# Kernel tuning notes

Measured on AMD Instinct MI355X. Metric: run time of the kernel, lower is better.

The kernel has to match this reference:

```python
import jax, jax.numpy as jnp
import numpy as np

SIZE_DICT = 512
DIM_DICT = 256
TEMPERATURE = 0.5
EPS = 1e-10


def setup_inputs() -> dict:
    key = jax.random.key(0)
    k1, k2, k3 = jax.random.split(key, 3)
    bs, dim_z, W, H = 32, DIM_DICT, 32, 32
    z_from_encoder = jax.random.normal(k1, (bs, dim_z, W, H), dtype=jnp.float32)
    kappa_q = jnp.ones((1,), dtype=jnp.float32)
    codebook = jax.random.normal(k2, (SIZE_DICT, DIM_DICT), dtype=jnp.float32)
    gumbel_u = jax.random.uniform(k3, (bs * W * H, SIZE_DICT), dtype=jnp.float32)
    return {"z_from_encoder": z_from_encoder, "kappa_q": kappa_q,
            "codebook": codebook, "gumbel_u": gumbel_u, "flg_train": 1}


def reference(z_from_encoder, kappa_q, codebook, gumbel_u, flg_train):
    bs, dim_z, W, H = z_from_encoder.shape
    # [bs, dim_z, W, H] -> [bs*W*H, dim_z]
    z_flat = jnp.transpose(z_from_encoder, (0, 2, 3, 1)).reshape(-1, dim_z)
    kq = jnp.clip(kappa_q, 1e-5, 1e5)  # scalar-ish [1]
    # L2-normalize codebook rows
    cb = codebook / jnp.linalg.norm(codebook, axis=1, keepdims=True)
    # logit = -distance = kappa * <z, c>   [N, K]
    logit = kq * (z_flat @ cb.T)
    logit = logit - jnp.max(logit, axis=-1, keepdims=True)
    logit = jnp.clip(logit, -50.0, 50.0)
    probabilities = jax.nn.softmax(logit, axis=-1)
    log_probabilities = jax.nn.log_softmax(logit, axis=-1)
    # training path: gumbel-softmax relaxation
    g = -jnp.log(-jnp.log(gumbel_u + EPS) + EPS)
    encodings = jax.nn.softmax((logit + g) / TEMPERATURE, axis=-1)
    z_quantized = (encodings @ cb).reshape(bs, W, H, dim_z)
    avg_probs = jnp.mean(jax.lax.stop_gradient(probabilities), axis=0)
    z_to_decoder = jnp.transpose(z_quantized, (0, 3, 1, 2))
    kld_discrete = jnp.sum(probabilities * log_probabilities) / bs
    kld_continuous = jnp.mean(
        jnp.sum(z_from_encoder * (z_from_encoder - z_to_decoder) * kq[0],
                axis=(1, 2, 3)))
    loss = kld_discrete + kld_continuous
    avg_probs = jnp.clip(avg_probs, 1e-10, None)
    perplexity = jnp.exp(-jnp.sum(avg_probs * jnp.log(avg_probs + 1e-10)))
    return z_to_decoder, loss, perplexity
```

## Files before the change

### kernel.cpp

```cpp
#include <hip/hip_runtime.h>
#include <stdint.h>


typedef float v4f __attribute__((ext_vector_type(4)));
typedef short v8s __attribute__((ext_vector_type(8)));
typedef short v4s __attribute__((ext_vector_type(4)));

#define ZA_STR 264
#define L2_STR 520

__device__ __forceinline__ uint16_t f2bf(float x) {
  uint32_t u = __float_as_uint(x);
  u = u + 0x7fffu + ((u >> 16) & 1u);
  return (uint16_t)(u >> 16);
}


__global__ __launch_bounds__(256) void vq_prep(const float* __restrict__ cb,
                                               const float* __restrict__ kappa,
                                               char* __restrict__ ws) {
  const int b = blockIdx.x, t = threadIdx.x;
  uint16_t* cbn2 = (uint16_t*)ws;
  uint16_t* cbt2 = (uint16_t*)(ws + 262144);
  float* shadow  = (float*)(ws + 524288);
  float* scal    = (float*)(ws + 557056);
  __shared__ float s_rn[8];

  const int cbase = (b & 63) << 3;
  const int cl = t >> 5, lt = t & 31;
  const float4 f0 = *(const float4*)(cb + (cbase + cl) * 256 + lt * 8);
  const float4 f1 = *(const float4*)(cb + (cbase + cl) * 256 + lt * 8 + 4);
  float s = f0.x*f0.x + f0.y*f0.y + f0.z*f0.z + f0.w*f0.w
          + f1.x*f1.x + f1.y*f1.y + f1.z*f1.z + f1.w*f1.w;
#pragma unroll
  for (int mm = 1; mm < 32; mm <<= 1) s += __shfl_xor(s, mm, 64);
  if (lt == 0) s_rn[cl] = 1.0f / sqrtf(s);
  __syncthreads();

  union { v8s v; uint16_t u[8]; } pk;
  if (b < 64) {
    const float kq = fminf(fmaxf(kappa[0], 1e-5f), 1e5f);
    const int code = cbase + cl, dch = lt;
    const float rn = s_rn[cl] * kq;
    pk.u[0] = f2bf(f0.x * rn); pk.u[1] = f2bf(f0.y * rn);
    pk.u[2] = f2bf(f0.z * rn); pk.u[3] = f2bf(f0.w * rn);
    pk.u[4] = f2bf(f1.x * rn); pk.u[5] = f2bf(f1.y * rn);
    pk.u[6] = f2bf(f1.z * rn); pk.u[7] = f2bf(f1.w * rn);
    const int w = code >> 7, ct = (code >> 4) & 7, mcol = code & 15;
    const int ks = dch >> 2, q3 = dch & 3;
    *(v8s*)(cbn2 + ((ks * 8 + ct) * 4 + w) * 512 + (q3 * 16 + mcol) * 8) = pk.v;
  } else {
    const int cgroup = b - 64, d = t;
#pragma unroll
    for (int j = 0; j < 8; j++) {
      const int c = cbase + j;
      pk.u[j] = f2bf(cb[c * 256 + d] * s_rn[j]);
    }
    const int cc = cgroup >> 2, qq = cgroup & 3;
    const int wd = d >> 6, nt = (d >> 4) & 3, md = d & 15;
    *(v8s*)(cbt2 + ((cc * 4 + nt) * 4 + wd) * 512 + (qq * 16 + md) * 8) = pk.v;
    if (t < 128) shadow[(cgroup << 7) + t] = 0.f;
    if (cgroup == 0 && t >= 128 && t < 131) scal[t - 128] = 0.f;
  }
}

__global__ __launch_bounds__(256, 4) void vq_main(const float* __restrict__ z,
                                                  const float* __restrict__ gum,
                                                  char* __restrict__ ws,
                                                  float* __restrict__ out) {
  __shared__ char s_A[33280];
  __shared__ float s_pm[128], s_pS[128], s_pT[128];
  __shared__ float s_M[32], s_rS[32], s_kd[32], s_rSe[32], s_red[8];
  __shared__ float s_se[128], s_ce[128];
  __shared__ float s_col[512];

  const int t = threadIdx.x;
  const int w = t >> 6, lane = t & 63, q = lane >> 4, m = lane & 15;
  const int bi = blockIdx.x, b = bi >> 5, wh0 = (bi & 31) << 5;
  const int R0 = bi << 5;

  const uint16_t* cbn2 = (const uint16_t*)ws;
  const uint16_t* cbt2 = (const uint16_t*)(ws + 262144);
  float* shadow = (float*)(ws + 524288);
  float* scal   = (float*)(ws + 557056);

  uint16_t* za  = (uint16_t*)s_A;
  uint16_t* l2s = (uint16_t*)s_A;

  {
    float zs = 0.f;
    const int whb = (t & 7) << 2, dT = t >> 3;
    const float* zb = z + ((size_t)b << 18) + wh0 + whb;
#pragma unroll
    for (int s = 0; s < 8; s++) {
      const int d = dT + (s << 5);
      const float4 v = *(const float4*)(zb + (d << 10));
      zs += v.x * v.x + v.y * v.y + v.z * v.z + v.w * v.w;
      za[(whb + 0) * ZA_STR + d] = f2bf(v.x);
      za[(whb + 1) * ZA_STR + d] = f2bf(v.y);
      za[(whb + 2) * ZA_STR + d] = f2bf(v.z);
      za[(whb + 3) * ZA_STR + d] = f2bf(v.w);
    }
#pragma unroll
    for (int mm = 1; mm < 64; mm <<= 1) zs += __shfl_xor(zs, mm, 64);
    if (lane == 0) s_red[w] = zs;
  }
  __syncthreads();
  if (t == 0) atomicAdd(&scal[1], s_red[0] + s_red[1] + s_red[2] + s_red[3]);

  v4f acc0[8], acc1[8];
#pragma unroll
  for (int i = 0; i < 8; i++) { acc0[i] = (v4f)0.f; acc1[i] = (v4f)0.f; }
  {
    const uint16_t* bp  = cbn2 + (w << 9) + (lane << 3);
    const uint16_t* a0p = za + m * ZA_STR;
    const uint16_t* a1p = za + (m + 16) * ZA_STR;
#pragma unroll
    for (int ks = 0; ks < 8; ks++) {
      const v8s a0 = *(const v8s*)(a0p + (ks << 5) + (q << 3));
      const v8s a1 = *(const v8s*)(a1p + (ks << 5) + (q << 3));
#pragma unroll
      for (int ct = 0; ct < 8; ct++) {
        const v8s bf = *(const v8s*)(bp + (((ks << 3) + ct) << 11));
        acc0[ct] = __builtin_amdgcn_mfma_f32_16x16x32_bf16(a0, bf, acc0[ct], 0, 0, 0);
        acc1[ct] = __builtin_amdgcn_mfma_f32_16x16x32_bf16(a1, bf, acc1[ct], 0, 0, 0);
      }
    }
  }

  {
    auto stats_half = [&](v4f (&acc)[8], int half) {
#pragma unroll
      for (int reg = 0; reg < 4; reg++) {
        float mx = -1e30f;
#pragma unroll
        for (int ct = 0; ct < 8; ct++) mx = fmaxf(mx, acc[ct][reg]);
#pragma unroll
        for (int mm = 1; mm < 16; mm <<= 1) mx = fmaxf(mx, __shfl_xor(mx, mm, 64));
        float S = 0.f, T = 0.f;
#pragma unroll
        for (int ct = 0; ct < 8; ct++) {
          const float d = acc[ct][reg] - mx;
          const float e = __expf(d);
          S += e; T += d * e;
        }
#pragma unroll
        for (int mm = 1; mm < 16; mm <<= 1) { S += __shfl_xor(S, mm, 64); T += __shfl_xor(T, mm, 64); }
        if (m == 0) {
          const int r = half * 16 + q * 4 + reg;
          s_pm[(w << 5) + r] = mx; s_pS[(w << 5) + r] = S; s_pT[(w << 5) + r] = T;
        }
      }
    };
    stats_half(acc0, 0);
    stats_half(acc1, 1);
  }

  const float* gT = gum + (((size_t)R0 + (q << 2)) << 9) + (w << 7) + m;
  float gb[2][8];
#pragma unroll
  for (int ct = 0; ct < 8; ct++) gb[0][ct] = gT[ct << 4];
#pragma unroll
  for (int ct = 0; ct < 8; ct++) gb[1][ct] = gT[512 + (ct << 4)];

  __syncthreads();
  if (t < 32) {
    float M = s_pm[t];
    M = fmaxf(M, s_pm[32 + t]); M = fmaxf(M, s_pm[64 + t]); M = fmaxf(M, s_pm[96 + t]);
    float S = 0.f, T = 0.f;
#pragma unroll
    for (int ww = 0; ww < 4; ww++) {
      const float dm = s_pm[ww * 32 + t] - M;
      const float al = __expf(dm);
      S += s_pS[ww * 32 + t] * al;
      T += (s_pT[ww * 32 + t] + dm * s_pS[ww * 32 + t]) * al;
    }
    const float rS = 1.0f / S;
    s_M[t] = M; s_rS[t] = rS; s_kd[t] = T * rS - __logf(S);
  }
  __syncthreads();

  {
    const int c0 = w << 7;
    float colacc[8];
#pragma unroll
    for (int i = 0; i < 8; i++) colacc[i] = 0.f;
#pragma unroll
    for (int g = 0; g < 8; g++) {
      const int h = g >> 2, rg = g & 3;
      const int r = (h << 4) + (q << 2) + rg;
      const float Mr = s_M[r], rSr = s_rS[r];
      uint16_t* lrow = l2s + r * L2_STR + c0 + m;
      float se = 0.f, ce = 0.f;
#pragma unroll
      for (int ct = 0; ct < 8; ct++) {
        const float a = h ? acc1[ct][rg] : acc0[ct][rg];
        const float d = fmaxf(a - Mr, -50.0f);
        const float e = __expf(d);
        colacc[ct] += e * rSr;
        const float L = 1e-10f - __logf(gb[g & 1][ct] + 1e-10f);
        const float f = __fdividef(e, L);
        const float er = f * f;
        se += er;
        ce += er * (d + Mr);
        lrow[ct << 4] = f2bf(er);
      }
      if (g < 6) {
        const int g2 = g + 2;
        const int off = (((g2 >> 2) << 4) + (g2 & 3)) << 9;
#pragma unroll
        for (int ct = 0; ct < 8; ct++) gb[g & 1][ct] = gT[off + (ct << 4)];
      }
#pragma unroll
      for (int mm = 1; mm < 16; mm <<= 1) {
        se += __shfl_xor(se, mm, 64);
        ce += __shfl_xor(ce, mm, 64);
      }
      if (m == 0) { s_se[(w << 5) + r] = se; s_ce[(w << 5) + r] = ce; }
    }
#pragma unroll
    for (int i = 0; i < 8; i++) {
      colacc[i] += __shfl_xor(colacc[i], 16, 64);
      colacc[i] += __shfl_xor(colacc[i], 32, 64);
    }
    if (q == 0) {
#pragma unroll
      for (int i = 0; i < 8; i++) s_col[c0 + (i << 4) + m] = colacc[i];
    }
  }
  __syncthreads();

  if (t < 32) {
    const float se = s_se[t] + s_se[32 + t] + s_se[64 + t] + s_se[96 + t];
    const float ce = s_ce[t] + s_ce[32 + t] + s_ce[64 + t] + s_ce[96 + t];
    s_rSe[t] = 1.0f / se;
    float cr = ce / se;
#pragma unroll
    for (int mm = 1; mm < 32; mm <<= 1) cr += __shfl_xor(cr, mm, 64);
    if (t == 0) atomicAdd(&scal[2], cr);
  }

  v4f acc2a[4], acc2b[4];
#pragma unroll
  for (int i = 0; i < 4; i++) { acc2a[i] = (v4f)0.f; acc2b[i] = (v4f)0.f; }
  {
    const uint16_t* a0p = l2s + m * L2_STR;
    const uint16_t* a1p = l2s + (m + 16) * L2_STR;
#pragma unroll
    for (int cc = 0; cc < 16; cc++) {
      const v8s a0 = *(const v8s*)(a0p + (cc << 5) + (q << 3));
      const v8s a1 = *(const v8s*)(a1p + (cc << 5) + (q << 3));
      const uint16_t* bp2 = cbt2 + (cc << 13) + (w << 9) + (lane << 3);
#pragma unroll
      for (int nt = 0; nt < 4; nt++) {
        const v8s bf = *(const v8s*)(bp2 + (nt << 11));
        acc2a[nt] = __builtin_amdgcn_mfma_f32_16x16x32_bf16(a0, bf, acc2a[nt], 0, 0, 0);
        acc2b[nt] = __builtin_amdgcn_mfma_f32_16x16x32_bf16(a1, bf, acc2b[nt], 0, 0, 0);
      }
    }
  }
  __syncthreads();

  {
    float* ob = out + ((size_t)b << 18) + wh0;
    const int d0 = w << 6;
    float rsA[4], rsB[4];
#pragma unroll
    for (int reg = 0; reg < 4; reg++) {
      rsA[reg] = s_rSe[q * 4 + reg];
      rsB[reg] = s_rSe[16 + q * 4 + reg];
    }
#pragma unroll
    for (int nt = 0; nt < 4; nt++) {
      const int d = d0 + (nt << 4) + m;
#pragma unroll
      for (int reg = 0; reg < 4; reg++) {
        ob[(d << 10) + q * 4 + reg]      = acc2a[nt][reg] * rsA[reg];
        ob[(d << 10) + 16 + q * 4 + reg] = acc2b[nt][reg] * rsB[reg];
      }
    }
  }

  {
    float* sh = shadow + ((bi & 15) << 9);
    atomicAdd(&sh[t], s_col[t]);
    atomicAdd(&sh[256 + t], s_col[256 + t]);
    if (w == 0) {
      float kd = s_kd[lane & 31];
#pragma unroll
      for (int mm = 1; mm < 64; mm <<= 1) kd += __shfl_xor(kd, mm, 64);
      if (lane == 0) atomicAdd(&scal[0], 0.5f * kd);
    }
  }
}

__global__ __launch_bounds__(512) void vq_final(const float* __restrict__ kappa,
                                                char* __restrict__ ws,
                                                float* __restrict__ out) {
  __shared__ float red[8];
  const int t = threadIdx.x;
  const float* shadow = (const float*)(ws + 524288);
  const float* scal   = (const float*)(ws + 557056);
  float s = 0.f;
#pragma unroll
  for (int j = 0; j < 16; j++) s += shadow[(j << 9) + t];
  float avg = fmaxf(s * (1.0f / 32768.0f), 1e-10f);
  float term = avg * __logf(avg + 1e-10f);
#pragma unroll
  for (int mm = 1; mm < 64; mm <<= 1) term += __shfl_xor(term, mm, 64);
  if ((t & 63) == 0) red[t >> 6] = term;
  __syncthreads();
  if (t == 0) {
    float H = 0.f;
#pragma unroll
    for (int i = 0; i < 8; i++) H += red[i];
    const float perpl = __expf(-H);
    const float kq = fminf(fmaxf(kappa[0], 1e-5f), 1e5f);
    const float loss = (scal[0] + kq * scal[1] - scal[2]) * (1.0f / 32.0f);
    out[8388608] = loss;
    out[8388609] = perpl;
  }
}

extern "C" void kernel_launch(void* const* d_in, const int* in_sizes, int n_in,
                              void* d_out, int out_size, void* d_ws, size_t ws_size,
                              hipStream_t stream) {
  const float* z     = (const float*)d_in[0];
  const float* kappa = (const float*)d_in[1];
  const float* cb    = (const float*)d_in[2];
  const float* gum   = (const float*)d_in[3];
  char* ws = (char*)d_ws;
  float* out = (float*)d_out;
  hipLaunchKernelGGL(vq_prep,  dim3(128),  dim3(256), 0, stream, cb, kappa, ws);
  hipLaunchKernelGGL(vq_main,  dim3(1024), dim3(256), 0, stream, z, gum, ws, out);
  hipLaunchKernelGGL(vq_final, dim3(1),    dim3(512), 0, stream, kappa, ws, out);
}
```

Measured before the change: 186.3 us.

## Permute codebook order for vectorized gumbel loads and fuse final reduction via last-block

Codes are permuted (pi_of) when building both codebook layouts, so each lane owns 8 contiguous codes. The gumbel noise can then be read with float4 loads instead of strided scalar loads. The separate final kernel is folded into vq_main using an atomic counter and last-block election, which removes a launch. One barrier is dropped by computing the per-row reciprocal sums inline. The risks are the counter being zeroed only in prep, added fence and atomic cost, and correctness that depends on the permutation being consistent between the two MFMA stages.

Result: slower. 385.1 us (+106.7%).

```diff
diff --git a/kernel.cpp b/kernel.cpp
--- a/kernel.cpp
+++ b/kernel.cpp
@@ -4,7 +4,6 @@
 
 typedef float v4f __attribute__((ext_vector_type(4)));
 typedef short v8s __attribute__((ext_vector_type(8)));
-typedef short v4s __attribute__((ext_vector_type(4)));
 
 #define ZA_STR 264
 #define L2_STR 520
@@ -13,6 +12,10 @@
   uint32_t u = __float_as_uint(x);
   u = u + 0x7fffu + ((u >> 16) & 1u);
   return (uint16_t)(u >> 16);
+}
+
+__device__ __forceinline__ int pi_of(int p) {
+  return ((p >> 7) << 7) + ((p & 15) << 3) + ((p >> 4) & 7);
 }
 
 
@@ -28,8 +31,9 @@
 
   const int cbase = (b & 63) << 3;
   const int cl = t >> 5, lt = t & 31;
-  const float4 f0 = *(const float4*)(cb + (cbase + cl) * 256 + lt * 8);
-  const float4 f1 = *(const float4*)(cb + (cbase + cl) * 256 + lt * 8 + 4);
+  const int crow = (b < 64) ? (cbase + cl) : pi_of(cbase + cl);
+  const float4 f0 = *(const float4*)(cb + crow * 256 + lt * 8);
+  const float4 f1 = *(const float4*)(cb + crow * 256 + lt * 8 + 4);
   float s = f0.x*f0.x + f0.y*f0.y + f0.z*f0.z + f0.w*f0.w
           + f1.x*f1.x + f1.y*f1.y + f1.z*f1.z + f1.w*f1.w;
 #pragma unroll
@@ -46,33 +50,35 @@
     pk.u[2] = f2bf(f0.z * rn); pk.u[3] = f2bf(f0.w * rn);
     pk.u[4] = f2bf(f1.x * rn); pk.u[5] = f2bf(f1.y * rn);
     pk.u[6] = f2bf(f1.z * rn); pk.u[7] = f2bf(f1.w * rn);
-    const int w = code >> 7, ct = (code >> 4) & 7, mcol = code & 15;
+    const int w = code >> 7, ct = code & 7, mcol = (code >> 3) & 15;
     const int ks = dch >> 2, q3 = dch & 3;
     *(v8s*)(cbn2 + ((ks * 8 + ct) * 4 + w) * 512 + (q3 * 16 + mcol) * 8) = pk.v;
   } else {
     const int cgroup = b - 64, d = t;
 #pragma unroll
     for (int j = 0; j < 8; j++) {
-      const int c = cbase + j;
-      pk.u[j] = f2bf(cb[c * 256 + d] * s_rn[j]);
+      const int code = pi_of((cgroup << 3) + j);
+      pk.u[j] = f2bf(cb[code * 256 + d] * s_rn[j]);
     }
     const int cc = cgroup >> 2, qq = cgroup & 3;
     const int wd = d >> 6, nt = (d >> 4) & 3, md = d & 15;
     *(v8s*)(cbt2 + ((cc * 4 + nt) * 4 + wd) * 512 + (qq * 16 + md) * 8) = pk.v;
     if (t < 128) shadow[(cgroup << 7) + t] = 0.f;
-    if (cgroup == 0 && t >= 128 && t < 131) scal[t - 128] = 0.f;
+    if (cgroup == 0 && t >= 128 && t < 132) scal[t - 128] = 0.f;
   }
 }
 
 __global__ __launch_bounds__(256, 4) void vq_main(const float* __restrict__ z,
+                                                  const float* __restrict__ kappa,
                                                   const float* __restrict__ gum,
                                                   char* __restrict__ ws,
                                                   float* __restrict__ out) {
   __shared__ char s_A[33280];
   __shared__ float s_pm[128], s_pS[128], s_pT[128];
-  __shared__ float s_M[32], s_rS[32], s_kd[32], s_rSe[32], s_red[8];
+  __shared__ float s_M[32], s_rS[32], s_kd[32], s_red[8];
   __shared__ float s_se[128], s_ce[128];
   __shared__ float s_col[512];
+  __shared__ int s_last;
 
   const int t = threadIdx.x;
   const int w = t >> 6, lane = t & 63, q = lane >> 4, m = lane & 15;
@@ -83,6 +89,7 @@
   const uint16_t* cbt2 = (const uint16_t*)(ws + 262144);
   float* shadow = (float*)(ws + 524288);
   float* scal   = (float*)(ws + 557056);
+  unsigned int* cnt = (unsigned int*)(ws + 557068);
 
   uint16_t* za  = (uint16_t*)s_A;
   uint16_t* l2s = (uint16_t*)s_A;
@@ -156,12 +163,11 @@
     stats_half(acc1, 1);
   }
 
-  const float* gT = gum + (((size_t)R0 + (q << 2)) << 9) + (w << 7) + m;
-  float gb[2][8];
-#pragma unroll
-  for (int ct = 0; ct < 8; ct++) gb[0][ct] = gT[ct << 4];
-#pragma unroll
-  for (int ct = 0; ct < 8; ct++) gb[1][ct] = gT[512 + (ct << 4)];
+  union GU { float4 v[2]; float f[8]; };
+  GU gA, gB;
+  const float* gT = gum + (((size_t)R0 + (q << 2)) << 9) + (w << 7) + (m << 3);
+  gA.v[0] = *(const float4*)(gT + 0);   gA.v[1] = *(const float4*)(gT + 4);
+  gB.v[0] = *(const float4*)(gT + 512); gB.v[1] = *(const float4*)(gT + 516);
 
   __syncthreads();
   if (t < 32) {
@@ -191,6 +197,7 @@
       const int r = (h << 4) + (q << 2) + rg;
       const float Mr = s_M[r], rSr = s_rS[r];
       uint16_t* lrow = l2s + r * L2_STR + c0 + m;
+      const GU& gu = (g & 1) ? gB : gA;
       float se = 0.f, ce = 0.f;
 #pragma unroll
       for (int ct = 0; ct < 8; ct++) {
@@ -198,7 +205,7 @@
         const float d = fmaxf(a - Mr, -50.0f);
         const float e = __expf(d);
         colacc[ct] += e * rSr;
-        const float L = 1e-10f - __logf(gb[g & 1][ct] + 1e-10f);
+        const float L = 1e-10f - __logf(gu.f[ct] + 1e-10f);
         const float f = __fdividef(e, L);
         const float er = f * f;
         se += er;
@@ -208,8 +215,9 @@
       if (g < 6) {
         const int g2 = g + 2;
         const int off = (((g2 >> 2) << 4) + (g2 & 3)) << 9;
-#pragma unroll
-        for (int ct = 0; ct < 8; ct++) gb[g & 1][ct] = gT[off + (ct << 4)];
+        GU& gw = (g & 1) ? gB : gA;
+        gw.v[0] = *(const float4*)(gT + off);
+        gw.v[1] = *(const float4*)(gT + off + 4);
       }
 #pragma unroll
       for (int mm = 1; mm < 16; mm <<= 1) {
@@ -229,16 +237,6 @@
     }
   }
   __syncthreads();
-
-  if (t < 32) {
-    const float se = s_se[t] + s_se[32 + t] + s_se[64 + t] + s_se[96 + t];
-    const float ce = s_ce[t] + s_ce[32 + t] + s_ce[64 + t] + s_ce[96 + t];
-    s_rSe[t] = 1.0f / se;
-    float cr = ce / se;
-#pragma unroll
-    for (int mm = 1; mm < 32; mm <<= 1) cr += __shfl_xor(cr, mm, 64);
-    if (t == 0) atomicAdd(&scal[2], cr);
-  }
 
   v4f acc2a[4], acc2b[4];
 #pragma unroll
@@ -259,7 +257,6 @@
       }
     }
   }
-  __syncthreads();
 
   {
     float* ob = out + ((size_t)b << 18) + wh0;
@@ -267,8 +264,9 @@
     float rsA[4], rsB[4];
 #pragma unroll
     for (int reg = 0; reg < 4; reg++) {
-      rsA[reg] = s_rSe[q * 4 + reg];
-      rsB[reg] = s_rSe[16 + q * 4 + reg];
+      const int rA = q * 4 + reg, rB = 16 + rA;
+      rsA[reg] = 1.0f / (s_se[rA] + s_se[32 + rA] + s_se[64 + rA] + s_se[96 + rA]);
+      rsB[reg] = 1.0f / (s_se[rB] + s_se[32 + rB] + s_se[64 + rB] + s_se[96 + rB]);
     }
 #pragma unroll
     for (int nt = 0; nt < 4; nt++) {
@@ -291,34 +289,50 @@
       for (int mm = 1; mm < 64; mm <<= 1) kd += __shfl_xor(kd, mm, 64);
       if (lane == 0) atomicAdd(&scal[0], 0.5f * kd);
     }
-  }
-}
-
-__global__ __launch_bounds__(512) void vq_final(const float* __restrict__ kappa,
-                                                char* __restrict__ ws,
-                                                float* __restrict__ out) {
-  __shared__ float red[8];
-  const int t = threadIdx.x;
-  const float* shadow = (const float*)(ws + 524288);
-  const float* scal   = (const float*)(ws + 557056);
-  float s = 0.f;
-#pragma unroll
-  for (int j = 0; j < 16; j++) s += shadow[(j << 9) + t];
-  float avg = fmaxf(s * (1.0f / 32768.0f), 1e-10f);
-  float term = avg * __logf(avg + 1e-10f);
-#pragma unroll
-  for (int mm = 1; mm < 64; mm <<= 1) term += __shfl_xor(term, mm, 64);
-  if ((t & 63) == 0) red[t >> 6] = term;
+    if (t < 32) {
+      const float se = s_se[t] + s_se[32 + t] + s_se[64 + t] + s_se[96 + t];
+      const float ce = s_ce[t] + s_ce[32 + t] + s_ce[64 + t] + s_ce[96 + t];
+      float cr = ce / se;
+#pragma unroll
+      for (int mm = 1; mm < 32; mm <<= 1) cr += __shfl_xor(cr, mm, 64);
+      if (t == 0) atomicAdd(&scal[2], cr);
+    }
+  }
+
+  __threadfence();
   __syncthreads();
   if (t == 0) {
-    float H = 0.f;
-#pragma unroll
-    for (int i = 0; i < 8; i++) H += red[i];
-    const float perpl = __expf(-H);
-    const float kq = fminf(fmaxf(kappa[0], 1e-5f), 1e5f);
-    const float loss = (scal[0] + kq * scal[1] - scal[2]) * (1.0f / 32.0f);
-    out[8388608] = loss;
-    out[8388609] = perpl;
+    const unsigned int old =
+        __hip_atomic_fetch_add(cnt, 1u, __ATOMIC_ACQ_REL, __HIP_MEMORY_SCOPE_AGENT);
+    s_last = (old == 1023u);
+  }
+  __syncthreads();
+  if (s_last) {
+    float term = 0.f;
+#pragma unroll
+    for (int ci = 0; ci < 2; ci++) {
+      const int c = t + (ci << 8);
+      float s = 0.f;
+#pragma unroll
+      for (int j = 0; j < 16; j++)
+        s += __hip_atomic_load(&shadow[(j << 9) + c], __ATOMIC_RELAXED,
+                               __HIP_MEMORY_SCOPE_AGENT);
+      const float avg = fmaxf(s * (1.0f / 32768.0f), 1e-10f);
+      term += avg * __logf(avg + 1e-10f);
+    }
+#pragma unroll
+    for (int mm = 1; mm < 64; mm <<= 1) term += __shfl_xor(term, mm, 64);
+    if (lane == 0) s_red[w] = term;
+    __syncthreads();
+    if (t == 0) {
+      const float H = s_red[0] + s_red[1] + s_red[2] + s_red[3];
+      const float s0 = __hip_atomic_load(&scal[0], __ATOMIC_RELAXED, __HIP_MEMORY_SCOPE_AGENT);
+      const float s1 = __hip_atomic_load(&scal[1], __ATOMIC_RELAXED, __HIP_MEMORY_SCOPE_AGENT);
+      const float s2 = __hip_atomic_load(&scal[2], __ATOMIC_RELAXED, __HIP_MEMORY_SCOPE_AGENT);
+      const float kq = fminf(fmaxf(kappa[0], 1e-5f), 1e5f);
+      out[8388608] = (s0 + kq * s1 - s2) * (1.0f / 32.0f);
+      out[8388609] = __expf(-H);
+    }
   }
 }
 
@@ -331,7 +345,6 @@
   const float* gum   = (const float*)d_in[3];
   char* ws = (char*)d_ws;
   float* out = (float*)d_out;
-  hipLaunchKernelGGL(vq_prep,  dim3(128),  dim3(256), 0, stream, cb, kappa, ws);
-  hipLaunchKernelGGL(vq_main,  dim3(1024), dim3(256), 0, stream, z, gum, ws, out);
-  hipLaunchKernelGGL(vq_final, dim3(1),    dim3(512), 0, stream, kappa, ws, out);
-}
+  hipLaunchKernelGGL(vq_prep, dim3(128),  dim3(256), 0, stream, cb, kappa, ws);
+  hipLaunchKernelGGL(vq_main, dim3(1024), dim3(256), 0, stream, z, kappa, gum, ws, out);
+}
```

## Permute codebook order so gumbel noise loads become vectorized float4 reads

Applied to the files above, without the earlier changes.

The codebook columns are permuted in the prep kernel (pi_of) so that each lane's 8 logit columns map to 8 contiguous gumbel entries. This lets the main kernel fetch gumbel noise with two float4 loads instead of eight strided scalar loads. The per-row softmax normaliser reduction is also folded into the output epilogue, which removes one block barrier and the s_rSe buffer. The permutation must stay consistent between the normalised codebook, its transpose and the column statistics, otherwise avg_probs would be computed in permuted order.

Measured after the change: 197.0 us. 1.06x slower.

```diff
diff --git a/kernel.cpp b/kernel.cpp
--- a/kernel.cpp
+++ b/kernel.cpp
@@ -4,7 +4,6 @@
 
 typedef float v4f __attribute__((ext_vector_type(4)));
 typedef short v8s __attribute__((ext_vector_type(8)));
-typedef short v4s __attribute__((ext_vector_type(4)));
 
 #define ZA_STR 264
 #define L2_STR 520
@@ -13,6 +12,10 @@
   uint32_t u = __float_as_uint(x);
   u = u + 0x7fffu + ((u >> 16) & 1u);
   return (uint16_t)(u >> 16);
+}
+
+__device__ __forceinline__ int pi_of(int p) {
+  return ((p >> 7) << 7) + ((p & 15) << 3) + ((p >> 4) & 7);
 }
 
 
@@ -28,8 +31,9 @@
 
   const int cbase = (b & 63) << 3;
   const int cl = t >> 5, lt = t & 31;
-  const float4 f0 = *(const float4*)(cb + (cbase + cl) * 256 + lt * 8);
-  const float4 f1 = *(const float4*)(cb + (cbase + cl) * 256 + lt * 8 + 4);
+  const int crow = (b < 64) ? (cbase + cl) : pi_of(cbase + cl);
+  const float4 f0 = *(const float4*)(cb + crow * 256 + lt * 8);
+  const float4 f1 = *(const float4*)(cb + crow * 256 + lt * 8 + 4);
   float s = f0.x*f0.x + f0.y*f0.y + f0.z*f0.z + f0.w*f0.w
           + f1.x*f1.x + f1.y*f1.y + f1.z*f1.z + f1.w*f1.w;
 #pragma unroll
@@ -46,15 +50,15 @@
     pk.u[2] = f2bf(f0.z * rn); pk.u[3] = f2bf(f0.w * rn);
     pk.u[4] = f2bf(f1.x * rn); pk.u[5] = f2bf(f1.y * rn);
     pk.u[6] = f2bf(f1.z * rn); pk.u[7] = f2bf(f1.w * rn);
-    const int w = code >> 7, ct = (code >> 4) & 7, mcol = code & 15;
+    const int w = code >> 7, ct = code & 7, mcol = (code >> 3) & 15;
     const int ks = dch >> 2, q3 = dch & 3;
     *(v8s*)(cbn2 + ((ks * 8 + ct) * 4 + w) * 512 + (q3 * 16 + mcol) * 8) = pk.v;
   } else {
     const int cgroup = b - 64, d = t;
 #pragma unroll
     for (int j = 0; j < 8; j++) {
-      const int c = cbase + j;
-      pk.u[j] = f2bf(cb[c * 256 + d] * s_rn[j]);
+      const int code = pi_of((cgroup << 3) + j);
+      pk.u[j] = f2bf(cb[code * 256 + d] * s_rn[j]);
     }
     const int cc = cgroup >> 2, qq = cgroup & 3;
     const int wd = d >> 6, nt = (d >> 4) & 3, md = d & 15;
@@ -70,7 +74,7 @@
                                                   float* __restrict__ out) {
   __shared__ char s_A[33280];
   __shared__ float s_pm[128], s_pS[128], s_pT[128];
-  __shared__ float s_M[32], s_rS[32], s_kd[32], s_rSe[32], s_red[8];
+  __shared__ float s_M[32], s_rS[32], s_kd[32], s_red[8];
   __shared__ float s_se[128], s_ce[128];
   __shared__ float s_col[512];
 
@@ -156,12 +160,11 @@
     stats_half(acc1, 1);
   }
 
-  const float* gT = gum + (((size_t)R0 + (q << 2)) << 9) + (w << 7) + m;
-  float gb[2][8];
-#pragma unroll
-  for (int ct = 0; ct < 8; ct++) gb[0][ct] = gT[ct << 4];
-#pragma unroll
-  for (int ct = 0; ct < 8; ct++) gb[1][ct] = gT[512 + (ct << 4)];
+  union GU { float4 v[2]; float f[8]; };
+  GU gA, gB;
+  const float* gT = gum + (((size_t)R0 + (q << 2)) << 9) + (w << 7) + (m << 3);
+  gA.v[0] = *(const float4*)(gT + 0);   gA.v[1] = *(const float4*)(gT + 4);
+  gB.v[0] = *(const float4*)(gT + 512); gB.v[1] = *(const float4*)(gT + 516);
 
   __syncthreads();
   if (t < 32) {
@@ -191,6 +194,7 @@
       const int r = (h << 4) + (q << 2) + rg;
       const float Mr = s_M[r], rSr = s_rS[r];
       uint16_t* lrow = l2s + r * L2_STR + c0 + m;
+      const GU& gu = (g & 1) ? gB : gA;
       float se = 0.f, ce = 0.f;
 #pragma unroll
       for (int ct = 0; ct < 8; ct++) {
@@ -198,7 +202,7 @@
         const float d = fmaxf(a - Mr, -50.0f);
         const float e = __expf(d);
         colacc[ct] += e * rSr;
-        const float L = 1e-10f - __logf(gb[g & 1][ct] + 1e-10f);
+        const float L = 1e-10f - __logf(gu.f[ct] + 1e-10f);
         const float f = __fdividef(e, L);
         const float er = f * f;
         se += er;
@@ -208,8 +212,9 @@
       if (g < 6) {
         const int g2 = g + 2;
         const int off = (((g2 >> 2) << 4) + (g2 & 3)) << 9;
-#pragma unroll
-        for (int ct = 0; ct < 8; ct++) gb[g & 1][ct] = gT[off + (ct << 4)];
+        GU& gw = (g & 1) ? gB : gA;
+        gw.v[0] = *(const float4*)(gT + off);
+        gw.v[1] = *(const float4*)(gT + off + 4);
       }
 #pragma unroll
       for (int mm = 1; mm < 16; mm <<= 1) {
@@ -229,16 +234,6 @@
     }
   }
   __syncthreads();
-
-  if (t < 32) {
-    const float se = s_se[t] + s_se[32 + t] + s_se[64 + t] + s_se[96 + t];
-    const float ce = s_ce[t] + s_ce[32 + t] + s_ce[64 + t] + s_ce[96 + t];
-    s_rSe[t] = 1.0f / se;
-    float cr = ce / se;
-#pragma unroll
-    for (int mm = 1; mm < 32; mm <<= 1) cr += __shfl_xor(cr, mm, 64);
-    if (t == 0) atomicAdd(&scal[2], cr);
-  }
 
   v4f acc2a[4], acc2b[4];
 #pragma unroll
@@ -259,7 +254,6 @@
       }
     }
   }
-  __syncthreads();
 
   {
     float* ob = out + ((size_t)b << 18) + wh0;
@@ -267,8 +261,9 @@
     float rsA[4], rsB[4];
 #pragma unroll
     for (int reg = 0; reg < 4; reg++) {
-      rsA[reg] = s_rSe[q * 4 + reg];
-      rsB[reg] = s_rSe[16 + q * 4 + reg];
+      const int rA = q * 4 + reg, rB = 16 + rA;
+      rsA[reg] = 1.0f / (s_se[rA] + s_se[32 + rA] + s_se[64 + rA] + s_se[96 + rA]);
+      rsB[reg] = 1.0f / (s_se[rB] + s_se[32 + rB] + s_se[64 + rB] + s_se[96 + rB]);
     }
 #pragma unroll
     for (int nt = 0; nt < 4; nt++) {
@@ -290,6 +285,14 @@
 #pragma unroll
       for (int mm = 1; mm < 64; mm <<= 1) kd += __shfl_xor(kd, mm, 64);
       if (lane == 0) atomicAdd(&scal[0], 0.5f * kd);
+    }
+    if (t < 32) {
+      const float se = s_se[t] + s_se[32 + t] + s_se[64 + t] + s_se[96 + t];
+      const float ce = s_ce[t] + s_ce[32 + t] + s_ce[64 + t] + s_ce[96 + t];
+      float cr = ce / se;
+#pragma unroll
+      for (int mm = 1; mm < 32; mm <<= 1) cr += __shfl_xor(cr, mm, 64);
+      if (t == 0) atomicAdd(&scal[2], cr);
     }
   }
 }
```
